# Performance work log

Measured on AMD Instinct MI355X. Metric: run time of the kernel, lower is better.

## Reference

```python
import jax, jax.numpy as jnp
import numpy as np

B, NF, N, D, S, H = 16, 16, 1024, 128, 8, 128
EPS = 1e-8
SCALE = D ** -0.5


def _ln(x, g, b):
    m = x.mean(-1, keepdims=True)
    v = ((x - m) ** 2).mean(-1, keepdims=True)
    return (x - m) / jnp.sqrt(v + 1e-5) * g + b


def setup_inputs() -> dict:
    key = jax.random.key(0)
    ks = jax.random.split(key, 16)
    w = lambda k, *s: jax.random.normal(k, s, jnp.float32) * 0.02
    return {
        'inputs': jax.random.normal(ks[0], (B, NF, N, D), jnp.float32),
        'slots_init': jax.random.normal(ks[1], (1, S, D), jnp.float32),
        'Wq': w(ks[2], D, D), 'bq': jnp.zeros((D,), jnp.float32),
        'Wk': w(ks[3], D, D), 'bk': jnp.zeros((D,), jnp.float32),
        'Wv': w(ks[4], D, D), 'bv': jnp.zeros((D,), jnp.float32),
        'W1': w(ks[5], H, D), 'b1': jnp.zeros((H,), jnp.float32),
        'W2': w(ks[6], D, H), 'b2': jnp.zeros((D,), jnp.float32),
        'Wih': w(ks[7], 3 * D, D), 'Whh': w(ks[8], 3 * D, D),
        'bih': jnp.zeros((3 * D,), jnp.float32), 'bhh': jnp.zeros((3 * D,), jnp.float32),
        'g_in': jnp.ones((D,), jnp.float32), 'be_in': jnp.zeros((D,), jnp.float32),
        'g_sl': jnp.ones((D,), jnp.float32), 'be_sl': jnp.zeros((D,), jnp.float32),
        'g_ff': jnp.ones((D,), jnp.float32), 'be_ff': jnp.zeros((D,), jnp.float32),
    }


def reference(inputs, slots_init, Wq, bq, Wk, bk, Wv, bv, W1, b1, W2, b2,
              Wih, Whh, bih, bhh, g_in, be_in, g_sl, be_sl, g_ff, be_ff):
    def gru(x, h):  # PyTorch GRUCell, x/h: [BS, D]
        gi = x @ Wih.T + bih
        gh = h @ Whh.T + bhh
        r = jax.nn.sigmoid(gi[:, :D] + gh[:, :D])
        z = jax.nn.sigmoid(gi[:, D:2 * D] + gh[:, D:2 * D])
        n = jnp.tanh(gi[:, 2 * D:] + r * gh[:, 2 * D:])
        return (1.0 - z) * n + z * h

    def get_attention(slots, x):  # slots [B,S,D], x [B,N,D]
        slots_prev = slots
        xn = _ln(x, g_in, be_in)
        k = xn @ Wk.T + bk
        v = xn @ Wv.T + bv
        q = _ln(slots, g_sl, be_sl) @ Wq.T + bq
        dots = jnp.einsum('bid,bjd->bij', q, k) * SCALE  # [B,S,N]
        attn_ori = jax.nn.softmax(dots, axis=1) + EPS    # softmax over slots
        attn = attn_ori / attn_ori.sum(axis=-1, keepdims=True)
        updates = jnp.einsum('bjd,bij->bid', v, attn)    # [B,S,D]
        slots = gru(updates.reshape(-1, D), slots_prev.reshape(-1, D)).reshape(slots.shape[0], -1, D)
        ff = jax.nn.relu(_ln(slots, g_ff, be_ff) @ W1.T + b1) @ W2.T + b2
        return slots + ff, attn_ori

    slots = jnp.broadcast_to(slots_init, (inputs.shape[0], S, D))
    slots, _ = get_attention(slots, inputs[:, 0])  # warm-up on frame 0

    def body(carry, x_f):
        s, a = get_attention(carry, x_f)
        return s, (s, a)

    _, (slots_seq, attn_seq) = jax.lax.scan(body, slots, jnp.moveaxis(inputs, 1, 0))
    slots_out = jnp.moveaxis(slots_seq, 0, 1)  # [B,NF,S,D]
    attns = jnp.moveaxis(attn_seq, 0, 1)       # [B,NF,S,N]
    return slots_out, attns
```

## Files before the change

kernel.cpp:

```cpp
#include <hip/hip_runtime.h>

#define B_ 16
#define NF_ 16
#define N_ 1024
#define D_ 128
#define S_ 8
#define SCALE_ 0.08838834764831845f
#define NB 256
#define NT 512

struct SmemA {
  float Xt[64 * 128];
  float at[8 * 64];
  float gqWs[1024];
  float mean[64], rinv[64];
  float c1s[8], c0s[8];
};
struct SmemB {
  float Pk[128];
  float gh[384];
  float gi[384];
  float hn[128], buf[128], hid[128], nrm[128];
  float red[16];
};

__device__ __forceinline__ float gload(const float* p) {
  return __hip_atomic_load(p, __ATOMIC_RELAXED, __HIP_MEMORY_SCOPE_AGENT);
}
__device__ __forceinline__ void gstore(float* p, float v) {
  __hip_atomic_store(p, v, __ATOMIC_RELAXED, __HIP_MEMORY_SCOPE_AGENT);
}
__device__ __forceinline__ void arrive(unsigned* c) {
  __syncthreads();
  if (threadIdx.x == 0) {
    __builtin_amdgcn_s_waitcnt(0);
    __hip_atomic_fetch_add(c, 1u, __ATOMIC_RELAXED, __HIP_MEMORY_SCOPE_AGENT);
  }
}
__device__ __forceinline__ void wait_for(unsigned* c, unsigned target) {
  if (threadIdx.x == 0) {
    while (__hip_atomic_load(c, __ATOMIC_RELAXED, __HIP_MEMORY_SCOPE_AGENT) < target)
      __builtin_amdgcn_s_sleep(1);
  }
  __syncthreads();
}

__device__ __forceinline__ float dot128f(const float* __restrict__ wrow, const float* x, float acc) {
  const float4* w = (const float4*)wrow;
#pragma unroll
  for (int i = 0; i < 32; ++i) {
    float4 v = w[i];
    const float4 xv = *(const float4*)(x + i * 4);
    acc += v.x * xv.x + v.y * xv.y + v.z * xv.z + v.w * xv.w;
  }
  return acc;
}

__device__ __forceinline__ void stats128(float v, int t, float* red, float& m, float& inv, float eps) {
  __syncthreads();
  float s = (t < 128) ? v : 0.f;
  float s2 = (t < 128) ? v * v : 0.f;
#pragma unroll
  for (int off = 32; off; off >>= 1) { s += __shfl_down(s, off); s2 += __shfl_down(s2, off); }
  if (t == 0)  { red[0] = s; red[2] = s2; }
  if (t == 64) { red[1] = s; red[3] = s2; }
  __syncthreads();
  m = (red[0] + red[1]) * (1.f / 128.f);
  float var = (red[2] + red[3]) * (1.f / 128.f) - m * m;
  inv = rsqrtf(var + 1e-5f);
}

__device__ __forceinline__ float sigm(float x) { return 1.f / (1.f + __expf(-x)); }
__device__ __forceinline__ float tanh_f(float x) { return 1.f - 2.f / (1.f + __expf(2.f * x)); }

__device__ __forceinline__ void stage_stats(const float4* pf, float* Xt, float* mean, float* rinv, int t) {
  float s1[4], s2[4];
#pragma unroll
  for (int i = 0; i < 4; ++i) {
    int r = (t >> 5) + i * 16, kg = t & 31;
    *(float4*)&Xt[r * 128 + ((kg ^ (r & 7)) << 2)] = pf[i];
    s1[i] = pf[i].x + pf[i].y + pf[i].z + pf[i].w;
    s2[i] = pf[i].x * pf[i].x + pf[i].y * pf[i].y + pf[i].z * pf[i].z + pf[i].w * pf[i].w;
  }
#pragma unroll
  for (int mk = 16; mk; mk >>= 1) {
#pragma unroll
    for (int i = 0; i < 4; ++i) { s1[i] += __shfl_xor(s1[i], mk); s2[i] += __shfl_xor(s2[i], mk); }
  }
  if ((t & 31) == 0) {
#pragma unroll
    for (int i = 0; i < 4; ++i) {
      int r = (t >> 5) + i * 16;
      float mm = s1[i] * (1.f / 128.f);
      mean[r] = mm;
      rinv[r] = rsqrtf(s2[i] * (1.f / 128.f) - mm * mm + 1e-5f);
    }
  }
}

__device__ void q_project_pub(SmemB& Bm, const float* slot,
    const float* __restrict__ g_sl, const float* __restrict__ be_sl,
    const float* __restrict__ Wqk, const float* __restrict__ bqk,
    const float* __restrict__ wqbk, const float* __restrict__ bqbk,
    const float* gI, const float* bI,
    float* gqW_g, float* cc_g, int b, int s, int t) {
  float m, inv;
  float sv = (t < 128) ? slot[t] : 0.f;
  stats128(sv, t, Bm.red, m, inv, 1e-5f);
  if (t < 128) Bm.nrm[t] = (sv - m) * inv * g_sl[t] + be_sl[t];
  __syncthreads();
  if (t < 128) {
    float qv = dot128f(Wqk + t * 128, Bm.nrm, bqk[t]);
    float gq = gI[t] * qv;
    gstore(&gqW_g[b * 1024 + s * 128 + t], gq);
    float r0 = gq, r1 = bI[t] * qv, r2 = wqbk[t] * Bm.nrm[t];
#pragma unroll
    for (int off = 32; off; off >>= 1) {
      r0 += __shfl_down(r0, off); r1 += __shfl_down(r1, off); r2 += __shfl_down(r2, off);
    }
    if ((t & 63) == 0) {
      int w = t >> 6;
      Bm.red[8 + w] = r0; Bm.red[10 + w] = r1; Bm.red[12 + w] = r2;
    }
  }
  __syncthreads();
  if (t == 0) {
    float c1 = Bm.red[8] + Bm.red[9];
    float qb = Bm.red[12] + Bm.red[13] + bqbk[0];
    float c0 = Bm.red[10] + Bm.red[11] + qb;
    gstore(&cc_g[b * 16 + s], c1);
    gstore(&cc_g[b * 16 + 8 + s], c0);
  }
}

__global__ __launch_bounds__(128) void precomp(
    const float* __restrict__ Wih, const float* __restrict__ bih,
    const float* __restrict__ Wv, const float* __restrict__ bv,
    const float* __restrict__ Wq, const float* __restrict__ bq,
    const float* __restrict__ Wk, const float* __restrict__ bk,
    float* Wiv, float* bihv, float* Wqk, float* bqk, float* wqbk, float* bqbk) {
  __shared__ float r2[2];
  int r = blockIdx.x, t = threadIdx.x;
  if (r < 384) {
    float acc = 0.f;
#pragma unroll 8
    for (int k = 0; k < 128; ++k) acc += Wih[r * 128 + k] * Wv[k * 128 + t];
    Wiv[r * 128 + t] = acc;
    float p = Wih[r * 128 + t] * bv[t];
#pragma unroll
    for (int off = 32; off; off >>= 1) p += __shfl_down(p, off);
    if ((t & 63) == 0) r2[t >> 6] = p;
    __syncthreads();
    if (t == 0) bihv[r] = r2[0] + r2[1] + bih[r];
  } else {
    int c = r - 384;
    float acc = 0.f;
#pragma unroll 8
    for (int dd = 0; dd < 128; ++dd) acc += Wk[dd * 128 + c] * Wq[dd * 128 + t];
    Wqk[c * 128 + t] = acc;
    float p = Wk[t * 128 + c] * bq[t];
#pragma unroll
    for (int off = 32; off; off >>= 1) p += __shfl_down(p, off);
    if ((t & 63) == 0) r2[t >> 6] = p;
    __syncthreads();
    if (t == 0) bqk[c] = r2[0] + r2[1];
    if (c == 0) {
      float a2 = 0.f;
#pragma unroll 8
      for (int dd = 0; dd < 128; ++dd) a2 += Wq[dd * 128 + t] * bk[dd];
      wqbk[t] = a2;
      float p2 = bq[t] * bk[t];
#pragma unroll
      for (int off = 32; off; off >>= 1) p2 += __shfl_down(p2, off);
      __syncthreads();
      if ((t & 63) == 0) r2[t >> 6] = p2;
      __syncthreads();
      if (t == 0) bqbk[0] = r2[0] + r2[1];
    }
  }
}

__global__ __launch_bounds__(NT) void slot_persist(
    const float* __restrict__ x, const float* __restrict__ slots_init,
    const float* __restrict__ Whh, const float* __restrict__ bhh,
    const float* __restrict__ W1, const float* __restrict__ b1,
    const float* __restrict__ W2, const float* __restrict__ b2,
    const float* __restrict__ g_in, const float* __restrict__ be_in,
    const float* __restrict__ g_sl, const float* __restrict__ be_sl,
    const float* __restrict__ g_ff, const float* __restrict__ be_ff,
    const float* __restrict__ Wiv, const float* __restrict__ bihv,
    const float* __restrict__ Wqk, const float* __restrict__ bqk,
    const float* __restrict__ wqbk, const float* __restrict__ bqbk,
    float* out_slots, float* out_attn,
    unsigned* cntA, unsigned* cntB,
    float* U_g, float* SMB_g, float* gqW_g, float* cc_g) {
  __shared__ __align__(16) SmemA sa;
  __shared__ __align__(16) SmemB sb;
  __shared__ __align__(16) float slot_sh[128];
  __shared__ __align__(16) float gs[128], bs_[128];
  int t = threadIdx.x, bid = blockIdx.x;
  int b = bid >> 4, jt = bid & 15;
  bool isB = (jt < 8);
  unsigned* cA = cntA + (b << 6);
  unsigned* cB = cntB + (b << 6);
  int s = t >> 6, j = t & 63;

  if (t < 128) { gs[t] = g_in[t]; bs_[t] = be_in[t]; }
  __syncthreads();
  if (isB) {
    if (t < 128) slot_sh[t] = slots_init[jt * 128 + t];
    q_project_pub(sb, slot_sh, g_sl, be_sl, Wqk, bqk, wqbk, bqbk, gs, bs_,
                  gqW_g, cc_g, b, jt, t);
    arrive(cB);
  }
  float4 pf[4];
  {
    const float* xsrc = x + (((long)b * NF_ + 0) * N_ + jt * 64) * D_;
#pragma unroll
    for (int i = 0; i < 4; ++i) {
      int ch = t + i * 512;
      pf[i] = *(const float4*)(xsrc + (ch >> 5) * 128 + (ch & 31) * 4);
    }
  }
  stage_stats(pf, sa.Xt, sa.mean, sa.rinv, t);

  for (int it = 0; it < 17; ++it) {
    int f = (it == 0) ? 0 : it - 1;
    int wo = it > 0;
    int par = it & 1;
    wait_for(cB, 8u * (it + 1));
    sa.gqWs[t] = gload(&gqW_g[b * 1024 + t]);
    sa.gqWs[512 + t] = gload(&gqW_g[b * 1024 + 512 + t]);
    if (t < 8) sa.c1s[t] = gload(&cc_g[b * 16 + t]);
    else if (t < 16) sa.c0s[t - 8] = gload(&cc_g[b * 16 + t]);
    __syncthreads();
    {
      const float4* qq4 = (const float4*)(sa.gqWs + s * 128);
      float d = 0.f;
#pragma unroll
      for (int k4 = 0; k4 < 32; ++k4) {
        float4 xv = *(const float4*)&sa.Xt[j * 128 + ((k4 ^ (j & 7)) << 2)];
        float4 qv = qq4[k4];
        d += xv.x * qv.x + xv.y * qv.y + xv.z * qv.z + xv.w * qv.w;
      }
      float val = (d - sa.mean[j] * sa.c1s[s]) * sa.rinv[j] + sa.c0s[s];
      sa.at[s * 64 + j] = val * SCALE_;
    }
    __syncthreads();
    if (t < 64) {
      float vals[8], mx = -1e30f;
#pragma unroll
      for (int ss = 0; ss < 8; ++ss) { vals[ss] = sa.at[ss * 64 + t]; mx = fmaxf(mx, vals[ss]); }
      float sum = 0.f;
#pragma unroll
      for (int ss = 0; ss < 8; ++ss) { vals[ss] = __expf(vals[ss] - mx); sum += vals[ss]; }
      float rr = 1.f / sum;
#pragma unroll
      for (int ss = 0; ss < 8; ++ss) { vals[ss] = vals[ss] * rr + 1e-8f; sa.at[ss * 64 + t] = vals[ss]; }
      if (wo) {
#pragma unroll
        for (int ss = 0; ss < 8; ++ss)
          out_attn[(((long)b * NF_ + f) * S_ + ss) * N_ + jt * 64 + t] = vals[ss];
      }
    }
    __syncthreads();
    {
      float v = sa.at[s * 64 + j];
      float vm = v * sa.mean[j] * sa.rinv[j];
#pragma unroll
      for (int off = 32; off; off >>= 1) { v += __shfl_down(v, off); vm += __shfl_down(vm, off); }
      if (j == 0) {
        float* smb = SMB_g + (b * 2 + par) * 16;
        atomicAdd(&smb[s], v);
        atomicAdd(&smb[8 + s], vm);
      }
    }
    {
      int k2 = t & 127, h = t >> 7;
      int dg = k2 >> 2, dr = k2 & 3;
      float u0 = 0.f, u1 = 0.f;
      const float* a0 = sa.at + h * 64;
      const float* a1 = sa.at + (h + 4) * 64;
#pragma unroll
      for (int j0 = 0; j0 < 64; j0 += 4) {
        float4 av0 = *(const float4*)(a0 + j0);
        float4 av1 = *(const float4*)(a1 + j0);
        float4 rv = *(const float4*)(sa.rinv + j0);
        float x0 = sa.Xt[(j0 + 0) * 128 + ((dg ^ ((j0 + 0) & 7)) << 2) + dr];
        float x1 = sa.Xt[(j0 + 1) * 128 + ((dg ^ ((j0 + 1) & 7)) << 2) + dr];
        float x2 = sa.Xt[(j0 + 2) * 128 + ((dg ^ ((j0 + 2) & 7)) << 2) + dr];
        float x3 = sa.Xt[(j0 + 3) * 128 + ((dg ^ ((j0 + 3) & 7)) << 2) + dr];
        float rx0 = rv.x * x0, rx1 = rv.y * x1, rx2 = rv.z * x2, rx3 = rv.w * x3;
        u0 += av0.x * rx0 + av0.y * rx1 + av0.z * rx2 + av0.w * rx3;
        u1 += av1.x * rx0 + av1.y * rx1 + av1.z * rx2 + av1.w * rx3;
      }
      float* Ub = U_g + ((b * 2 + par) << 10);
      atomicAdd(&Ub[h * 128 + k2], u0);
      atomicAdd(&Ub[(h + 4) * 128 + k2], u1);
    }
    arrive(cA);
    if (isB) {
      wait_for(cA, 16u * (it + 1));
      int sl = jt;
      float* Ub = U_g + ((b * 2 + par) << 10);
      float* smb = SMB_g + (b * 2 + par) * 16;
      if (t < 128) {
        sb.Pk[t] = gload(&Ub[sl * 128 + t]);
        if (t == 0) {
          sb.red[14] = gload(&smb[sl]);
          sb.red[15] = gload(&smb[8 + sl]);
        }
      } else {
        int r = t - 128;
        sb.gh[r] = dot128f(Whh + r * 128, slot_sh, bhh[r]);
      }
      __syncthreads();
      float ssv = sb.red[14], mbv = sb.red[15];
      if (t < 128) {
        sb.Pk[t] = gs[t] * (sb.Pk[t] - mbv) + bs_[t] * ssv;
        gstore(&Ub[sl * 128 + t], 0.f);
        if (t == 0) { gstore(&smb[sl], 0.f); gstore(&smb[8 + sl], 0.f); }
      }
      __syncthreads();
      if (t < 384) sb.gi[t] = dot128f(Wiv + (long)t * 128, sb.Pk, 0.f);
      __syncthreads();
      float hnew = 0.f;
      if (t < 128) {
        float invss = 1.f / ssv;
        float gr = sigm(sb.gi[t] * invss + bihv[t] + sb.gh[t]);
        float gz = sigm(sb.gi[128 + t] * invss + bihv[128 + t] + sb.gh[128 + t]);
        float gn = tanh_f(sb.gi[256 + t] * invss + bihv[256 + t] + gr * sb.gh[256 + t]);
        hnew = (1.f - gz) * gn + gz * slot_sh[t];
        sb.hn[t] = hnew;
      }
      float m, inv;
      stats128(hnew, t, sb.red, m, inv, 1e-5f);
      if (t < 128) sb.buf[t] = (hnew - m) * inv * g_ff[t] + be_ff[t];
      __syncthreads();
      if (t < 128) sb.hid[t] = fmaxf(dot128f(W1 + t * 128, sb.buf, b1[t]), 0.f);
      __syncthreads();
      if (t < 128) {
        float ffv = dot128f(W2 + t * 128, sb.hid, b2[t]);
        float sn = sb.hn[t] + ffv;
        slot_sh[t] = sn;
        if (wo) out_slots[(((long)b * NF_ + f) * S_ + sl) * D_ + t] = sn;
      }
      __syncthreads();
      if (it < 16) {
        q_project_pub(sb, slot_sh, g_sl, be_sl, Wqk, bqk, wqbk, bqbk, gs, bs_,
                      gqW_g, cc_g, b, sl, t);
        arrive(cB);
      }
    }
    if (it < 16) {
      const float* xsrc = x + (((long)b * NF_ + it) * N_ + jt * 64) * D_;
#pragma unroll
      for (int i = 0; i < 4; ++i) {
        int ch = t + i * 512;
        pf[i] = *(const float4*)(xsrc + (ch >> 5) * 128 + (ch & 31) * 4);
      }
      stage_stats(pf, sa.Xt, sa.mean, sa.rinv, t);
    }
  }
}

extern "C" void kernel_launch(void* const* d_in, const int* in_sizes, int n_in,
                              void* d_out, int out_size, void* d_ws, size_t ws_size,
                              hipStream_t stream) {
  const float* inputs     = (const float*)d_in[0];
  const float* slots_init = (const float*)d_in[1];
  const float* Wq  = (const float*)d_in[2];
  const float* bq  = (const float*)d_in[3];
  const float* Wk  = (const float*)d_in[4];
  const float* bk  = (const float*)d_in[5];
  const float* Wv  = (const float*)d_in[6];
  const float* bv  = (const float*)d_in[7];
  const float* W1  = (const float*)d_in[8];
  const float* b1  = (const float*)d_in[9];
  const float* W2  = (const float*)d_in[10];
  const float* b2  = (const float*)d_in[11];
  const float* Wih = (const float*)d_in[12];
  const float* Whh = (const float*)d_in[13];
  const float* bih = (const float*)d_in[14];
  const float* bhh = (const float*)d_in[15];
  const float* g_in  = (const float*)d_in[16];
  const float* be_in = (const float*)d_in[17];
  const float* g_sl  = (const float*)d_in[18];
  const float* be_sl = (const float*)d_in[19];
  const float* g_ff  = (const float*)d_in[20];
  const float* be_ff = (const float*)d_in[21];

  float* out_slots = (float*)d_out;
  float* out_attn  = out_slots + (size_t)B_ * NF_ * S_ * D_;

  char* ws = (char*)d_ws;
  unsigned* cntA = (unsigned*)ws;
  unsigned* cntB = (unsigned*)(ws + 4096);
  float* U_g   = (float*)(ws + 8192);
  float* SMB_g = (float*)(ws + 139264);
  float* Wiv   = (float*)(ws + 141312);
  float* bihv  = (float*)(ws + 337920);
  float* WqkW  = (float*)(ws + 339456);
  float* bqk   = (float*)(ws + 404992);
  float* wqbk  = (float*)(ws + 405504);
  float* bqbk  = (float*)(ws + 406016);
  float* gqW_g = (float*)(ws + 406272);
  float* cc_g  = (float*)(ws + 471808);

  hipMemsetAsync(d_ws, 0, 141312, stream);

  precomp<<<512, 128, 0, stream>>>(Wih, bih, Wv, bv, Wq, bq, Wk, bk,
                                   Wiv, bihv, WqkW, bqk, wqbk, bqbk);
  slot_persist<<<NB, NT, 0, stream>>>(inputs, slots_init, Whh, bhh,
      W1, b1, W2, b2, g_in, be_in, g_sl, be_sl, g_ff, be_ff,
      Wiv, bihv, WqkW, bqk, wqbk, bqbk,
      out_slots, out_attn, cntA, cntB, U_g, SMB_g, gqW_g, cc_g);
}
```

Measured before the change: 712.2 us.

## Normalize inputs during staging and split slot-block matvecs across all threads

The input LayerNorm (including gamma/beta) is now applied while staging each frame into shared memory. This removes the mean/rinv correction terms from the dot products, the value aggregation and the GRU input path, and the scale is folded into the published query. The per-slot matvecs (q projection, Wiv, W1, W2) now use all 512 threads with four lanes per row, shuffle reductions and padded shared vectors, where before only 128 or 384 threads worked. Attention and slot output stores are moved after the arrive signal so they sit off the critical path, and the extra per-frame reductions and atomics are dropped. A redundant reload of frame 0 at iteration 1 is skipped, at the cost of more normalization arithmetic per staged element.

Result: faster. 663.3 us (-6.9%).

```diff
diff --git a/kernel.cpp b/kernel.cpp
--- a/kernel.cpp
+++ b/kernel.cpp
@@ -8,19 +8,20 @@
 #define SCALE_ 0.08838834764831845f
 #define NB 256
 #define NT 512
+#define CPAD(i) ((((i) >> 5) * 36) + ((i) & 31))
 
 struct SmemA {
   float Xt[64 * 128];
   float at[8 * 64];
-  float gqWs[1024];
-  float mean[64], rinv[64];
-  float c1s[8], c0s[8];
+  float qWs[1024];
+  float qbs[8];
 };
 struct SmemB {
-  float Pk[128];
+  float Uk[144];
   float gh[384];
   float gi[384];
-  float hn[128], buf[128], hid[128], nrm[128];
+  float hn[128];
+  float buf[144], hid[144], nrm[144];
   float red[16];
 };
 
@@ -73,12 +74,11 @@
 __device__ __forceinline__ float sigm(float x) { return 1.f / (1.f + __expf(-x)); }
 __device__ __forceinline__ float tanh_f(float x) { return 1.f - 2.f / (1.f + __expf(2.f * x)); }
 
-__device__ __forceinline__ void stage_stats(const float4* pf, float* Xt, float* mean, float* rinv, int t) {
+__device__ __forceinline__ void stage_norm(const float4* pf, float* Xt,
+                                           float4 g4, float4 b4, int t) {
   float s1[4], s2[4];
 #pragma unroll
   for (int i = 0; i < 4; ++i) {
-    int r = (t >> 5) + i * 16, kg = t & 31;
-    *(float4*)&Xt[r * 128 + ((kg ^ (r & 7)) << 2)] = pf[i];
     s1[i] = pf[i].x + pf[i].y + pf[i].z + pf[i].w;
     s2[i] = pf[i].x * pf[i].x + pf[i].y * pf[i].y + pf[i].z * pf[i].z + pf[i].w * pf[i].w;
   }
@@ -87,14 +87,18 @@
 #pragma unroll
     for (int i = 0; i < 4; ++i) { s1[i] += __shfl_xor(s1[i], mk); s2[i] += __shfl_xor(s2[i], mk); }
   }
-  if ((t & 31) == 0) {
-#pragma unroll
-    for (int i = 0; i < 4; ++i) {
-      int r = (t >> 5) + i * 16;
-      float mm = s1[i] * (1.f / 128.f);
-      mean[r] = mm;
-      rinv[r] = rsqrtf(s2[i] * (1.f / 128.f) - mm * mm + 1e-5f);
-    }
+  int kg = t & 31;
+#pragma unroll
+  for (int i = 0; i < 4; ++i) {
+    int r = (t >> 5) + i * 16;
+    float m = s1[i] * (1.f / 128.f);
+    float inv = rsqrtf(s2[i] * (1.f / 128.f) - m * m + 1e-5f);
+    float4 v = pf[i];
+    v.x = (v.x - m) * inv * g4.x + b4.x;
+    v.y = (v.y - m) * inv * g4.y + b4.y;
+    v.z = (v.z - m) * inv * g4.z + b4.z;
+    v.w = (v.w - m) * inv * g4.w + b4.w;
+    *(float4*)&Xt[r * 128 + ((kg ^ (r & 7)) << 2)] = v;
   }
 }
 
@@ -102,35 +106,34 @@
     const float* __restrict__ g_sl, const float* __restrict__ be_sl,
     const float* __restrict__ Wqk, const float* __restrict__ bqk,
     const float* __restrict__ wqbk, const float* __restrict__ bqbk,
-    const float* gI, const float* bI,
-    float* gqW_g, float* cc_g, int b, int s, int t) {
+    float* qW_g, float* qb_g, int b, int sl, int t) {
   float m, inv;
   float sv = (t < 128) ? slot[t] : 0.f;
   stats128(sv, t, Bm.red, m, inv, 1e-5f);
-  if (t < 128) Bm.nrm[t] = (sv - m) * inv * g_sl[t] + be_sl[t];
+  if (t < 128) {
+    float nv = (sv - m) * inv * g_sl[t] + be_sl[t];
+    Bm.nrm[CPAD(t)] = nv;
+    float qp = wqbk[t] * nv;
+#pragma unroll
+    for (int off = 32; off; off >>= 1) qp += __shfl_down(qp, off);
+    if (t == 0)  Bm.red[4] = qp;
+    if (t == 64) Bm.red[5] = qp;
+  }
   __syncthreads();
-  if (t < 128) {
-    float qv = dot128f(Wqk + t * 128, Bm.nrm, bqk[t]);
-    float gq = gI[t] * qv;
-    gstore(&gqW_g[b * 1024 + s * 128 + t], gq);
-    float r0 = gq, r1 = bI[t] * qv, r2 = wqbk[t] * Bm.nrm[t];
-#pragma unroll
-    for (int off = 32; off; off >>= 1) {
-      r0 += __shfl_down(r0, off); r1 += __shfl_down(r1, off); r2 += __shfl_down(r2, off);
-    }
-    if ((t & 63) == 0) {
-      int w = t >> 6;
-      Bm.red[8 + w] = r0; Bm.red[10 + w] = r1; Bm.red[12 + w] = r2;
-    }
-  }
-  __syncthreads();
-  if (t == 0) {
-    float c1 = Bm.red[8] + Bm.red[9];
-    float qb = Bm.red[12] + Bm.red[13] + bqbk[0];
-    float c0 = Bm.red[10] + Bm.red[11] + qb;
-    gstore(&cc_g[b * 16 + s], c1);
-    gstore(&cc_g[b * 16 + 8 + s], c0);
-  }
+  {
+    int c = t & 3, r = t >> 2;
+    const float4* wr = (const float4*)(Wqk + r * 128 + c * 32);
+    float acc = 0.f;
+#pragma unroll
+    for (int q = 0; q < 8; ++q) {
+      float4 wv = wr[q];
+      float4 vv = *(const float4*)&Bm.nrm[c * 36 + q * 4];
+      acc += wv.x * vv.x + wv.y * vv.y + wv.z * vv.z + wv.w * vv.w;
+    }
+    acc += __shfl_down(acc, 2); acc += __shfl_down(acc, 1);
+    if (c == 0) gstore(&qW_g[b * 1024 + sl * 128 + r], (acc + bqk[r]) * SCALE_);
+  }
+  if (t == 0) gstore(&qb_g[b * 8 + sl], (Bm.red[4] + Bm.red[5] + bqbk[0]) * SCALE_);
 }
 
 __global__ __launch_bounds__(128) void precomp(
@@ -193,11 +196,10 @@
     const float* __restrict__ wqbk, const float* __restrict__ bqbk,
     float* out_slots, float* out_attn,
     unsigned* cntA, unsigned* cntB,
-    float* U_g, float* SMB_g, float* gqW_g, float* cc_g) {
+    float* U_g, float* SS_g, float* qW_g, float* qb_g) {
   __shared__ __align__(16) SmemA sa;
   __shared__ __align__(16) SmemB sb;
   __shared__ __align__(16) float slot_sh[128];
-  __shared__ __align__(16) float gs[128], bs_[128];
   int t = threadIdx.x, bid = blockIdx.x;
   int b = bid >> 4, jt = bid & 15;
   bool isB = (jt < 8);
@@ -205,12 +207,12 @@
   unsigned* cB = cntB + (b << 6);
   int s = t >> 6, j = t & 63;
 
-  if (t < 128) { gs[t] = g_in[t]; bs_[t] = be_in[t]; }
-  __syncthreads();
+  const float4 g4 = *(const float4*)(g_in + (t & 31) * 4);
+  const float4 b4 = *(const float4*)(be_in + (t & 31) * 4);
+
   if (isB) {
     if (t < 128) slot_sh[t] = slots_init[jt * 128 + t];
-    q_project_pub(sb, slot_sh, g_sl, be_sl, Wqk, bqk, wqbk, bqbk, gs, bs_,
-                  gqW_g, cc_g, b, jt, t);
+    q_project_pub(sb, slot_sh, g_sl, be_sl, Wqk, bqk, wqbk, bqbk, qW_g, qb_g, b, jt, t);
     arrive(cB);
   }
   float4 pf[4];
@@ -222,20 +224,19 @@
       pf[i] = *(const float4*)(xsrc + (ch >> 5) * 128 + (ch & 31) * 4);
     }
   }
-  stage_stats(pf, sa.Xt, sa.mean, sa.rinv, t);
+  stage_norm(pf, sa.Xt, g4, b4, t);
 
   for (int it = 0; it < 17; ++it) {
     int f = (it == 0) ? 0 : it - 1;
     int wo = it > 0;
     int par = it & 1;
     wait_for(cB, 8u * (it + 1));
-    sa.gqWs[t] = gload(&gqW_g[b * 1024 + t]);
-    sa.gqWs[512 + t] = gload(&gqW_g[b * 1024 + 512 + t]);
-    if (t < 8) sa.c1s[t] = gload(&cc_g[b * 16 + t]);
-    else if (t < 16) sa.c0s[t - 8] = gload(&cc_g[b * 16 + t]);
+    sa.qWs[t] = gload(&qW_g[b * 1024 + t]);
+    sa.qWs[512 + t] = gload(&qW_g[b * 1024 + 512 + t]);
+    if (t < 8) sa.qbs[t] = gload(&qb_g[b * 8 + t]);
     __syncthreads();
     {
-      const float4* qq4 = (const float4*)(sa.gqWs + s * 128);
+      const float4* qq4 = (const float4*)(sa.qWs + s * 128);
       float d = 0.f;
 #pragma unroll
       for (int k4 = 0; k4 < 32; ++k4) {
@@ -243,12 +244,12 @@
         float4 qv = qq4[k4];
         d += xv.x * qv.x + xv.y * qv.y + xv.z * qv.z + xv.w * qv.w;
       }
-      float val = (d - sa.mean[j] * sa.c1s[s]) * sa.rinv[j] + sa.c0s[s];
-      sa.at[s * 64 + j] = val * SCALE_;
+      sa.at[s * 64 + j] = d + sa.qbs[s];
     }
     __syncthreads();
+    float vals[8];
     if (t < 64) {
-      float vals[8], mx = -1e30f;
+      float mx = -1e30f;
 #pragma unroll
       for (int ss = 0; ss < 8; ++ss) { vals[ss] = sa.at[ss * 64 + t]; mx = fmaxf(mx, vals[ss]); }
       float sum = 0.f;
@@ -257,23 +258,13 @@
       float rr = 1.f / sum;
 #pragma unroll
       for (int ss = 0; ss < 8; ++ss) { vals[ss] = vals[ss] * rr + 1e-8f; sa.at[ss * 64 + t] = vals[ss]; }
-      if (wo) {
-#pragma unroll
-        for (int ss = 0; ss < 8; ++ss)
-          out_attn[(((long)b * NF_ + f) * S_ + ss) * N_ + jt * 64 + t] = vals[ss];
-      }
     }
     __syncthreads();
     {
       float v = sa.at[s * 64 + j];
-      float vm = v * sa.mean[j] * sa.rinv[j];
-#pragma unroll
-      for (int off = 32; off; off >>= 1) { v += __shfl_down(v, off); vm += __shfl_down(vm, off); }
-      if (j == 0) {
-        float* smb = SMB_g + (b * 2 + par) * 16;
-        atomicAdd(&smb[s], v);
-        atomicAdd(&smb[8 + s], vm);
-      }
+#pragma unroll
+      for (int off = 32; off; off >>= 1) v += __shfl_down(v, off);
+      if (j == 0) atomicAdd(&SS_g[(b * 2 + par) * 8 + s], v);
     }
     {
       int k2 = t & 127, h = t >> 7;
@@ -285,48 +276,61 @@
       for (int j0 = 0; j0 < 64; j0 += 4) {
         float4 av0 = *(const float4*)(a0 + j0);
         float4 av1 = *(const float4*)(a1 + j0);
-        float4 rv = *(const float4*)(sa.rinv + j0);
         float x0 = sa.Xt[(j0 + 0) * 128 + ((dg ^ ((j0 + 0) & 7)) << 2) + dr];
         float x1 = sa.Xt[(j0 + 1) * 128 + ((dg ^ ((j0 + 1) & 7)) << 2) + dr];
         float x2 = sa.Xt[(j0 + 2) * 128 + ((dg ^ ((j0 + 2) & 7)) << 2) + dr];
         float x3 = sa.Xt[(j0 + 3) * 128 + ((dg ^ ((j0 + 3) & 7)) << 2) + dr];
-        float rx0 = rv.x * x0, rx1 = rv.y * x1, rx2 = rv.z * x2, rx3 = rv.w * x3;
-        u0 += av0.x * rx0 + av0.y * rx1 + av0.z * rx2 + av0.w * rx3;
-        u1 += av1.x * rx0 + av1.y * rx1 + av1.z * rx2 + av1.w * rx3;
+        u0 += av0.x * x0 + av0.y * x1 + av0.z * x2 + av0.w * x3;
+        u1 += av1.x * x0 + av1.y * x1 + av1.z * x2 + av1.w * x3;
       }
       float* Ub = U_g + ((b * 2 + par) << 10);
       atomicAdd(&Ub[h * 128 + k2], u0);
       atomicAdd(&Ub[(h + 4) * 128 + k2], u1);
     }
     arrive(cA);
+    if (wo && t < 64) {
+#pragma unroll
+      for (int ss = 0; ss < 8; ++ss)
+        out_attn[(((long)b * NF_ + f) * S_ + ss) * N_ + jt * 64 + t] = vals[ss];
+    }
     if (isB) {
       wait_for(cA, 16u * (it + 1));
       int sl = jt;
-      float* Ub = U_g + ((b * 2 + par) << 10);
-      float* smb = SMB_g + (b * 2 + par) * 16;
+      float* Ub = U_g + ((b * 2 + par) << 10) + sl * 128;
+      float* ssb = SS_g + (b * 2 + par) * 8;
       if (t < 128) {
-        sb.Pk[t] = gload(&Ub[sl * 128 + t]);
-        if (t == 0) {
-          sb.red[14] = gload(&smb[sl]);
-          sb.red[15] = gload(&smb[8 + sl]);
-        }
+        float uv = gload(&Ub[t]);
+        sb.Uk[CPAD(t)] = uv;
+        gstore(&Ub[t], 0.f);
+        if (t == 0) { sb.red[14] = gload(&ssb[sl]); gstore(&ssb[sl], 0.f); }
       } else {
         int r = t - 128;
-        sb.gh[r] = dot128f(Whh + r * 128, slot_sh, bhh[r]);
-      }
-      __syncthreads();
-      float ssv = sb.red[14], mbv = sb.red[15];
-      if (t < 128) {
-        sb.Pk[t] = gs[t] * (sb.Pk[t] - mbv) + bs_[t] * ssv;
-        gstore(&Ub[sl * 128 + t], 0.f);
-        if (t == 0) { gstore(&smb[sl], 0.f); gstore(&smb[8 + sl], 0.f); }
-      }
-      __syncthreads();
-      if (t < 384) sb.gi[t] = dot128f(Wiv + (long)t * 128, sb.Pk, 0.f);
+        sb.gh[r] = dot128f(Whh + (long)r * 128, slot_sh, bhh[r]);
+      }
+      __syncthreads();
+      {
+        int c = t & 3, rb = t >> 2;
+        float4 uv[8];
+#pragma unroll
+        for (int q = 0; q < 8; ++q) uv[q] = *(const float4*)&sb.Uk[c * 36 + q * 4];
+#pragma unroll
+        for (int g = 0; g < 3; ++g) {
+          int r = rb + g * 128;
+          const float4* wr = (const float4*)(Wiv + (long)r * 128 + c * 32);
+          float acc = 0.f;
+#pragma unroll
+          for (int q = 0; q < 8; ++q) {
+            float4 wv = wr[q];
+            acc += wv.x * uv[q].x + wv.y * uv[q].y + wv.z * uv[q].z + wv.w * uv[q].w;
+          }
+          acc += __shfl_down(acc, 2); acc += __shfl_down(acc, 1);
+          if (c == 0) sb.gi[r] = acc;
+        }
+      }
       __syncthreads();
       float hnew = 0.f;
       if (t < 128) {
-        float invss = 1.f / ssv;
+        float invss = 1.f / sb.red[14];
         float gr = sigm(sb.gi[t] * invss + bihv[t] + sb.gh[t]);
         float gz = sigm(sb.gi[128 + t] * invss + bihv[128 + t] + sb.gh[128 + t]);
         float gn = tanh_f(sb.gi[256 + t] * invss + bihv[256 + t] + gr * sb.gh[256 + t]);
@@ -335,31 +339,52 @@
       }
       float m, inv;
       stats128(hnew, t, sb.red, m, inv, 1e-5f);
-      if (t < 128) sb.buf[t] = (hnew - m) * inv * g_ff[t] + be_ff[t];
-      __syncthreads();
-      if (t < 128) sb.hid[t] = fmaxf(dot128f(W1 + t * 128, sb.buf, b1[t]), 0.f);
-      __syncthreads();
-      if (t < 128) {
-        float ffv = dot128f(W2 + t * 128, sb.hid, b2[t]);
-        float sn = sb.hn[t] + ffv;
-        slot_sh[t] = sn;
-        if (wo) out_slots[(((long)b * NF_ + f) * S_ + sl) * D_ + t] = sn;
-      }
-      __syncthreads();
+      if (t < 128) sb.buf[CPAD(t)] = (hnew - m) * inv * g_ff[t] + be_ff[t];
+      __syncthreads();
+      {
+        int c = t & 3, r = t >> 2;
+        const float4* wr = (const float4*)(W1 + r * 128 + c * 32);
+        float acc = 0.f;
+#pragma unroll
+        for (int q = 0; q < 8; ++q) {
+          float4 wv = wr[q];
+          float4 vv = *(const float4*)&sb.buf[c * 36 + q * 4];
+          acc += wv.x * vv.x + wv.y * vv.y + wv.z * vv.z + wv.w * vv.w;
+        }
+        acc += __shfl_down(acc, 2); acc += __shfl_down(acc, 1);
+        if (c == 0) sb.hid[CPAD(r)] = fmaxf(acc + b1[r], 0.f);
+      }
+      __syncthreads();
+      {
+        int c = t & 3, r = t >> 2;
+        const float4* wr = (const float4*)(W2 + r * 128 + c * 32);
+        float acc = 0.f;
+#pragma unroll
+        for (int q = 0; q < 8; ++q) {
+          float4 wv = wr[q];
+          float4 vv = *(const float4*)&sb.hid[c * 36 + q * 4];
+          acc += wv.x * vv.x + wv.y * vv.y + wv.z * vv.z + wv.w * vv.w;
+        }
+        acc += __shfl_down(acc, 2); acc += __shfl_down(acc, 1);
+        if (c == 0) slot_sh[r] = sb.hn[r] + acc + b2[r];
+      }
       if (it < 16) {
-        q_project_pub(sb, slot_sh, g_sl, be_sl, Wqk, bqk, wqbk, bqbk, gs, bs_,
-                      gqW_g, cc_g, b, sl, t);
+        q_project_pub(sb, slot_sh, g_sl, be_sl, Wqk, bqk, wqbk, bqbk, qW_g, qb_g, b, sl, t);
         arrive(cB);
-      }
-    }
-    if (it < 16) {
+      } else {
+        __syncthreads();
+      }
+      if (wo && t < 128)
+        out_slots[(((long)b * NF_ + f) * S_ + sl) * D_ + t] = slot_sh[t];
+    }
+    if (it && it < 16) {
       const float* xsrc = x + (((long)b * NF_ + it) * N_ + jt * 64) * D_;
 #pragma unroll
       for (int i = 0; i < 4; ++i) {
         int ch = t + i * 512;
         pf[i] = *(const float4*)(xsrc + (ch >> 5) * 128 + (ch & 31) * 4);
       }
-      stage_stats(pf, sa.Xt, sa.mean, sa.rinv, t);
+      stage_norm(pf, sa.Xt, g4, b4, t);
     }
   }
 }
@@ -397,22 +422,22 @@
   unsigned* cntA = (unsigned*)ws;
   unsigned* cntB = (unsigned*)(ws + 4096);
   float* U_g   = (float*)(ws + 8192);
-  float* SMB_g = (float*)(ws + 139264);
-  float* Wiv   = (float*)(ws + 141312);
-  float* bihv  = (float*)(ws + 337920);
-  float* WqkW  = (float*)(ws + 339456);
-  float* bqk   = (float*)(ws + 404992);
-  float* wqbk  = (float*)(ws + 405504);
-  float* bqbk  = (float*)(ws + 406016);
-  float* gqW_g = (float*)(ws + 406272);
-  float* cc_g  = (float*)(ws + 471808);
-
-  hipMemsetAsync(d_ws, 0, 141312, stream);
+  float* SS_g  = (float*)(ws + 139264);
+  float* Wiv   = (float*)(ws + 140288);
+  float* bihv  = (float*)(ws + 336896);
+  float* WqkW  = (float*)(ws + 338432);
+  float* bqk   = (float*)(ws + 403968);
+  float* wqbk  = (float*)(ws + 404480);
+  float* bqbk  = (float*)(ws + 404992);
+  float* qW_g  = (float*)(ws + 405248);
+  float* qb_g  = (float*)(ws + 470784);
+
+  hipMemsetAsync(d_ws, 0, 140288, stream);
 
   precomp<<<512, 128, 0, stream>>>(Wih, bih, Wv, bv, Wq, bq, Wk, bk,
                                    Wiv, bihv, WqkW, bqk, wqbk, bqbk);
   slot_persist<<<NB, NT, 0, stream>>>(inputs, slots_init, Whh, bhh,
       W1, b1, W2, b2, g_in, be_in, g_sl, be_sl, g_ff, be_ff,
       Wiv, bihv, WqkW, bqk, wqbk, bqbk,
-      out_slots, out_attn, cntA, cntB, U_g, SMB_g, gqW_g, cc_g);
-}
+      out_slots, out_attn, cntA, cntB, U_g, SS_g, qW_g, qb_g);
+}
```
